# Optimization experiments

Measured on AMD Instinct MI355X. Metric: run time of the kernel, lower is better.

Reference implementation:

```python
import jax, jax.numpy as jnp
import numpy as np

DIM = 1028


def setup_inputs() -> dict:
    key = jax.random.key(0)
    ks = jax.random.split(key, 11)
    B, N = 8, 2048
    s = 0.02
    x = jax.random.normal(ks[0], (B, N, DIM), dtype=jnp.float32)
    Wq = jax.random.normal(ks[1], (DIM, DIM), dtype=jnp.float32) * s
    bq = jax.random.normal(ks[2], (DIM,), dtype=jnp.float32) * s
    Wk = jax.random.normal(ks[3], (DIM, DIM), dtype=jnp.float32) * s
    bk = jax.random.normal(ks[4], (DIM,), dtype=jnp.float32) * s
    Wv = jax.random.normal(ks[5], (DIM, DIM), dtype=jnp.float32) * s
    bv = jax.random.normal(ks[6], (DIM,), dtype=jnp.float32) * s
    We = jax.random.normal(ks[7], (4 * DIM, DIM), dtype=jnp.float32) * s
    be = jax.random.normal(ks[8], (4 * DIM,), dtype=jnp.float32) * s
    Wo = jax.random.normal(ks[9], (DIM, 4 * DIM), dtype=jnp.float32) * s
    bo = jax.random.normal(ks[10], (DIM,), dtype=jnp.float32) * s
    return {"x": x, "Wq": Wq, "bq": bq, "Wk": Wk, "bk": bk, "Wv": Wv,
            "bv": bv, "We": We, "be": be, "Wo": Wo, "bo": bo}


def reference(x, Wq, bq, Wk, bk, Wv, bv, We, be, Wo, bo):
    # x: [B, N, D]. torch Linear weight is [out, in] -> x @ W.T + b
    q = jnp.einsum('bnd,ed->bne', x, Wq) + bq
    k = jnp.einsum('bnd,ed->bne', x, Wk) + bk
    v = jnp.einsum('bnd,ed->bne', x, Wv) + bv
    scores = jnp.einsum('bqd,bkd->bqk', q, k) / jnp.sqrt(jnp.float32(DIM))
    w = jax.nn.softmax(scores, axis=-1)          # [B, N, N]
    attn = jnp.einsum('bqk,bkd->bqd', w, v)      # [B, N, D]
    h = jax.nn.gelu(jnp.einsum('bnd,hd->bnh', attn, We) + be, approximate=False)
    out = jnp.einsum('bnh,dh->bnd', h, Wo) + bo
    return out + x
```

## Files before the change

### kernel.cpp

```cpp
#include <hip/hip_runtime.h>
#include <hip/hip_bf16.h>
#include <cstdint>
#include <cmath>


typedef __bf16 bf16;
typedef __bf16 bf16x8 __attribute__((ext_vector_type(8)));
typedef float  f32x4  __attribute__((ext_vector_type(4)));

#define D_REAL   1028
#define D_PADK   1088
#define D_PADN   1152
#define H_REAL   4112
#define H_PAD    4224
#define NTOK     2048
#define NB       8
#define MTOT     (NB*NTOK)
#define SLAB_X   ((size_t)NTOK*D_PADK)
#define SLAB_S   ((size_t)NTOK*NTOK)
#define WSLAB    ((size_t)D_PADN*D_PADK)
#define VSLAB    ((size_t)D_PADN*NTOK)

__device__ __forceinline__ void async16(const void* g, void* l) {
    __builtin_amdgcn_global_load_lds(
        (__attribute__((address_space(1))) void*)(uintptr_t)g,
        (__attribute__((address_space(3))) void*)(uint32_t)(uintptr_t)l,
        16, 0, 0);
}

template <int EPI, bool XPIN>
__global__ __launch_bounds__(256)
void gemm_bt(const bf16* __restrict__ A, size_t strideA,
             const bf16* __restrict__ B, size_t strideB,
             const float* __restrict__ bias, size_t strideBias,
             void* __restrict__ Out, size_t strideOut,
             bf16* __restrict__ OutV,
             int K, int outPitch, int colBound, float scale,
             const float* __restrict__ resid)
{
    __shared__ __attribute__((aligned(16))) bf16 tA[128 * 64];
    __shared__ __attribute__((aligned(16))) bf16 tB[128 * 64];

    int bx, by, bz;
    if (XPIN) { bz = blockIdx.x; by = blockIdx.y; bx = blockIdx.z; }
    else      { bx = blockIdx.x; by = blockIdx.y; bz = blockIdx.z; }

    A += (size_t)bz * strideA;
    B += (size_t)bz * strideB;
    if (bias) bias += (size_t)bz * strideBias;

    const int tid  = threadIdx.x;
    const int lane = tid & 63;
    const int wv   = tid >> 6;
    const int wm   = wv >> 1;
    const int wn   = wv & 1;

    f32x4 acc[4][4] = {};

    const int sRow = lane >> 3;
    const int sCh  = (lane & 7) ^ sRow;
    const bf16* gA = A + (size_t)(by * 128 + wv * 32 + sRow) * K + sCh * 8;
    const bf16* gB = B + (size_t)(bx * 128 + wv * 32 + sRow) * K + sCh * 8;
    bf16* lA = &tA[(wv * 32) * 64];
    bf16* lB = &tB[(wv * 32) * 64];

    const int lr  = lane & 15;
    const int lq  = lane >> 4;
    const int rsw = lr & 7;

    for (int k0 = 0; k0 < K; k0 += 64) {
        async16(gA,                  lA);
        async16(gA + (size_t) 8 * K, lA +  8 * 64);
        async16(gA + (size_t)16 * K, lA + 16 * 64);
        async16(gA + (size_t)24 * K, lA + 24 * 64);
        async16(gB,                  lB);
        async16(gB + (size_t) 8 * K, lB +  8 * 64);
        async16(gB + (size_t)16 * K, lB + 16 * 64);
        async16(gB + (size_t)24 * K, lB + 24 * 64);
        gA += 64; gB += 64;
        __syncthreads();

        #pragma unroll
        for (int kk = 0; kk < 2; ++kk) {
            const int sl = ((kk * 4 + lq) ^ rsw) << 3;
            bf16x8 af[4], bfr[4];
            #pragma unroll
            for (int i = 0; i < 4; ++i) {
                af[i]  = *(const bf16x8*)&tA[(wm * 64 + i * 16 + lr) * 64 + sl];
                bfr[i] = *(const bf16x8*)&tB[(wn * 64 + i * 16 + lr) * 64 + sl];
            }
            #pragma unroll
            for (int i = 0; i < 4; ++i)
                #pragma unroll
                for (int j = 0; j < 4; ++j)
                    acc[i][j] = __builtin_amdgcn_mfma_f32_16x16x32_bf16(
                        af[i], bfr[j], acc[i][j], 0, 0, 0);
        }
        __syncthreads();
    }

    #pragma unroll
    for (int i = 0; i < 4; ++i) {
        #pragma unroll
        for (int j = 0; j < 4; ++j) {
            f32x4 v = acc[i][j];
            const int cg = bx * 128 + wn * 64 + j * 16 + lr;
            if (cg >= colBound) continue;
            const int rowBase = by * 128 + wm * 64 + i * 16 + lq * 4;
            const float bs = bias ? bias[cg] : 0.0f;
            #pragma unroll
            for (int r = 0; r < 4; ++r) {
                const int mg = rowBase + r;
                const float val = v[r];
                if (EPI == 0) {
                    ((bf16*)Out + (size_t)bz * strideOut)[(size_t)mg * outPitch + cg] =
                        (bf16)(val + bs);
                } else if (EPI == 3) {
                    const float u = val + bs;
                    const float g = 0.5f * u * (1.0f + erff(u * 0.70710678118654752f));
                    ((bf16*)Out)[(size_t)mg * outPitch + cg] = (bf16)g;
                } else if (EPI == 4) {
                    ((float*)Out)[(size_t)mg * outPitch + cg] =
                        val + bs + resid[(size_t)mg * outPitch + cg];
                } else if (EPI == 5) {
                    const int grp = cg / D_PADN;
                    const int c   = cg - grp * D_PADN;
                    const float u = val + bs;
                    if (grp < 2) {
                        if (c < D_PADK)
                            ((bf16*)Out)[(size_t)bz * 2 * SLAB_X + (size_t)grp * SLAB_X +
                                         (size_t)mg * D_PADK + c] = (bf16)u;
                    } else {
                        OutV[(size_t)bz * VSLAB + (size_t)c * NTOK + mg] = (bf16)u;
                    }
                } else {
                    ((bf16*)Out + (size_t)bz * strideOut)[(size_t)mg * outPitch + cg] =
                        (bf16)(val * scale);
                }
            }
        }
    }
}

__global__ __launch_bounds__(256)
void cvt_pad(const float* __restrict__ src, int R, int C,
             bf16* __restrict__ dst, int CP)
{
    const int c = blockIdx.x * 256 + threadIdx.x;
    const int r = blockIdx.y;
    if (c >= CP) return;
    const float v = (r < R && c < C) ? src[(size_t)r * C + c] : 0.0f;
    dst[(size_t)r * CP + c] = (bf16)v;
}

__global__ __launch_bounds__(256)
void pad_bias(const float* __restrict__ src, int n, float* __restrict__ dst, int np)
{
    const int i = blockIdx.x * 256 + threadIdx.x;
    if (i < np) dst[i] = (i < n) ? src[i] : 0.0f;
}

__global__ __launch_bounds__(256)
void softmax_ip(bf16* __restrict__ S)
{
    const int row  = blockIdx.x * 4 + (threadIdx.x >> 6);
    const int lane = threadIdx.x & 63;
    bf16* s = S + (size_t)row * NTOK + lane * 8;

    float v[32];
    #pragma unroll
    for (int j = 0; j < 4; ++j) {
        bf16x8 t = *(const bf16x8*)(s + j * 512);
        #pragma unroll
        for (int e = 0; e < 8; ++e) v[j * 8 + e] = (float)t[e];
    }
    float m = -1e30f;
    #pragma unroll
    for (int i = 0; i < 32; ++i) m = fmaxf(m, v[i]);
    #pragma unroll
    for (int off = 32; off > 0; off >>= 1) m = fmaxf(m, __shfl_xor(m, off, 64));

    float sum = 0.0f;
    #pragma unroll
    for (int i = 0; i < 32; ++i) { v[i] = __expf(v[i] - m); sum += v[i]; }
    #pragma unroll
    for (int off = 32; off > 0; off >>= 1) sum += __shfl_xor(sum, off, 64);
    const float inv = 1.0f / sum;

    #pragma unroll
    for (int j = 0; j < 4; ++j) {
        bf16x8 t;
        #pragma unroll
        for (int e = 0; e < 8; ++e) t[e] = (bf16)(v[j * 8 + e] * inv);
        *(bf16x8*)(s + j * 512) = t;
    }
}

#define OFF_WQKV   0u
#define OFF_WE     7520256u
#define OFF_WO     16711680u
#define OFF_BQKV   26443776u
#define OFF_BE     26457600u
#define OFF_XBF    26474496u
#define OFF_VT     62126080u
#define OFF_SCR    99874816u
#define QS_BYTES   8912896u
#define SS_BYTES   8388608u

extern "C" void kernel_launch(void* const* d_in, const int* in_sizes, int n_in,
                              void* d_out, int out_size, void* d_ws, size_t ws_size,
                              hipStream_t stream)
{
    const float* x  = (const float*)d_in[0];
    const float* Wq = (const float*)d_in[1];
    const float* bq = (const float*)d_in[2];
    const float* Wk = (const float*)d_in[3];
    const float* bk = (const float*)d_in[4];
    const float* Wv = (const float*)d_in[5];
    const float* bv = (const float*)d_in[6];
    const float* We = (const float*)d_in[7];
    const float* be = (const float*)d_in[8];
    const float* Wo = (const float*)d_in[9];
    const float* bo = (const float*)d_in[10];

    char* ws = (char*)d_ws;
    bf16*  Wqkv = (bf16*)(ws + OFF_WQKV);
    bf16*  WeP  = (bf16*)(ws + OFF_WE);
    bf16*  WoP  = (bf16*)(ws + OFF_WO);
    float* Bqkv = (float*)(ws + OFF_BQKV);
    float* BeP  = (float*)(ws + OFF_BE);
    bf16*  Xbf  = (bf16*)(ws + OFF_XBF);
    bf16*  Vt   = (bf16*)(ws + OFF_VT);
    char*  scr  = ws + OFF_SCR;

    const size_t avail = ws_size > OFF_SCR ? ws_size - OFF_SCR : 0;
    const size_t perG  = (size_t)QS_BYTES + SS_BYTES;
    int G = (avail >= 8 * perG) ? 8 : (avail >= 4 * perG) ? 4
          : (avail >= 2 * perG) ? 2 : 1;
    int R = (avail >= 69206016u) ? 8192 : (avail >= 34603008u) ? 4096 : 2048;

    bf16* Qs = (bf16*)scr;
    bf16* Ss = (bf16*)(scr + (size_t)G * QS_BYTES);
    bf16* Hb = (bf16*)scr;

    const dim3 blk(256);
    const float inv_sqrt_d = (float)(1.0 / sqrt((double)D_REAL));

    cvt_pad<<<dim3(5, MTOT), blk, 0, stream>>>(x, MTOT, D_REAL, Xbf, D_PADK);
    cvt_pad<<<dim3(5, D_PADN), blk, 0, stream>>>(Wq, D_REAL, D_REAL, Wqkv, D_PADK);
    cvt_pad<<<dim3(5, D_PADN), blk, 0, stream>>>(Wk, D_REAL, D_REAL, Wqkv + WSLAB, D_PADK);
    cvt_pad<<<dim3(5, D_PADN), blk, 0, stream>>>(Wv, D_REAL, D_REAL, Wqkv + 2 * WSLAB, D_PADK);
    cvt_pad<<<dim3(5, H_PAD), blk, 0, stream>>>(We, H_REAL, D_REAL, WeP, D_PADK);
    cvt_pad<<<dim3(17, D_PADN), blk, 0, stream>>>(Wo, D_REAL, H_REAL, WoP, H_PAD);
    pad_bias<<<dim3(5), blk, 0, stream>>>(bq, D_REAL, Bqkv, D_PADN);
    pad_bias<<<dim3(5), blk, 0, stream>>>(bk, D_REAL, Bqkv + D_PADN, D_PADN);
    pad_bias<<<dim3(5), blk, 0, stream>>>(bv, D_REAL, Bqkv + 2 * D_PADN, D_PADN);
    pad_bias<<<dim3(17), blk, 0, stream>>>(be, H_REAL, BeP, H_PAD);

    for (int g0 = 0; g0 < NB; g0 += G) {
        gemm_bt<5, false><<<dim3(27, 16, G), blk, 0, stream>>>(
            Xbf + (size_t)g0 * SLAB_X, SLAB_X, Wqkv, 0, Bqkv, 0,
            Qs, 0, Vt + (size_t)g0 * VSLAB,
            D_PADK, 0, 3456, 1.0f, nullptr);
        gemm_bt<6, true><<<dim3(G, 16, 16), blk, 0, stream>>>(
            Qs, 2 * SLAB_X, Qs + SLAB_X, 2 * SLAB_X, nullptr, 0,
            Ss, SLAB_S, nullptr, D_PADK, NTOK, NTOK, inv_sqrt_d, nullptr);
        softmax_ip<<<dim3(G * 512), blk, 0, stream>>>(Ss);
        gemm_bt<0, true><<<dim3(G, 16, 9), blk, 0, stream>>>(
            Ss, SLAB_S, Vt + (size_t)g0 * VSLAB, VSLAB, nullptr, 0,
            Xbf + (size_t)g0 * SLAB_X, SLAB_X, nullptr,
            NTOK, D_PADK, D_PADK, 1.0f, nullptr);
    }

    for (int r0 = 0; r0 < MTOT; r0 += R) {
        gemm_bt<3, false><<<dim3(33, R / 128, 1), blk, 0, stream>>>(
            Xbf + (size_t)r0 * D_PADK, 0, WeP, 0, BeP, 0,
            Hb, 0, nullptr, D_PADK, H_PAD, H_PAD, 1.0f, nullptr);
        gemm_bt<4, false><<<dim3(9, R / 128, 1), blk, 0, stream>>>(
            Hb, 0, WoP, 0, bo, 0,
            (float*)d_out + (size_t)r0 * D_REAL, 0, nullptr,
            H_PAD, D_REAL, D_REAL, 1.0f, x + (size_t)r0 * D_REAL);
    }
}
```

Before: 1.069 ms.

## Replace 128x128 GEMM with 256x256 double-buffered 512-thread pipelined kernel

Replaces the single-buffered 128x128 GEMM with a 256x256 tile kernel that runs 8 waves. It double-buffers A and B in LDS, issues async global-to-LDS loads for later k-tiles between MFMA phases, and raises wave priority during MFMA bursts. Non-pinned grids also get an XCD-aware block remap. The aim is more reuse of each loaded tile, and hiding load latency behind MFMA work. In exchange it uses 128KB of LDS per block, which limits occupancy. Edge tiles read past padded weight and V rows, relying on column guards to discard the results.

```diff
diff --git a/kernel.cpp b/kernel.cpp
--- a/kernel.cpp
+++ b/kernel.cpp
@@ -28,9 +28,11 @@
         16, 0, 0);
 }
 
+#define MFMA_(a, b, c) __builtin_amdgcn_mfma_f32_16x16x32_bf16(a, b, c, 0, 0, 0)
+
 template <int EPI, bool XPIN>
-__global__ __launch_bounds__(256)
-void gemm_bt(const bf16* __restrict__ A, size_t strideA,
+__global__ __launch_bounds__(512, 2)
+void gemm256(const bf16* __restrict__ A, size_t strideA,
              const bf16* __restrict__ B, size_t strideB,
              const float* __restrict__ bias, size_t strideBias,
              void* __restrict__ Out, size_t strideOut,
@@ -38,12 +40,19 @@
              int K, int outPitch, int colBound, float scale,
              const float* __restrict__ resid)
 {
-    __shared__ __attribute__((aligned(16))) bf16 tA[128 * 64];
-    __shared__ __attribute__((aligned(16))) bf16 tB[128 * 64];
+    __shared__ __attribute__((aligned(16))) bf16 sAB[4][256 * 64];
 
     int bx, by, bz;
-    if (XPIN) { bz = blockIdx.x; by = blockIdx.y; bx = blockIdx.z; }
-    else      { bx = blockIdx.x; by = blockIdx.y; bz = blockIdx.z; }
+    if (XPIN) {
+        bz = blockIdx.x; by = blockIdx.y; bx = blockIdx.z;
+    } else {
+        const int nx   = gridDim.x;
+        const int nwg  = nx * gridDim.y;
+        const int orig = blockIdx.y * nx + blockIdx.x;
+        const int q    = nwg >> 3;
+        const int wg   = (orig & 7) * q + (orig >> 3);
+        bx = wg % nx; by = wg / nx; bz = blockIdx.z;
+    }
 
     A += (size_t)bz * strideA;
     B += (size_t)bz * strideB;
@@ -52,61 +61,127 @@
     const int tid  = threadIdx.x;
     const int lane = tid & 63;
     const int wv   = tid >> 6;
-    const int wm   = wv >> 1;
-    const int wn   = wv & 1;
-
-    f32x4 acc[4][4] = {};
-
-    const int sRow = lane >> 3;
-    const int sCh  = (lane & 7) ^ sRow;
-    const bf16* gA = A + (size_t)(by * 128 + wv * 32 + sRow) * K + sCh * 8;
-    const bf16* gB = B + (size_t)(bx * 128 + wv * 32 + sRow) * K + sCh * 8;
-    bf16* lA = &tA[(wv * 32) * 64];
-    bf16* lB = &tB[(wv * 32) * 64];
-
-    const int lr  = lane & 15;
-    const int lq  = lane >> 4;
-    const int rsw = lr & 7;
-
-    for (int k0 = 0; k0 < K; k0 += 64) {
-        async16(gA,                  lA);
-        async16(gA + (size_t) 8 * K, lA +  8 * 64);
-        async16(gA + (size_t)16 * K, lA + 16 * 64);
-        async16(gA + (size_t)24 * K, lA + 24 * 64);
-        async16(gB,                  lB);
-        async16(gB + (size_t) 8 * K, lB +  8 * 64);
-        async16(gB + (size_t)16 * K, lB + 16 * 64);
-        async16(gB + (size_t)24 * K, lB + 24 * 64);
-        gA += 64; gB += 64;
-        __syncthreads();
-
-        #pragma unroll
-        for (int kk = 0; kk < 2; ++kk) {
-            const int sl = ((kk * 4 + lq) ^ rsw) << 3;
-            bf16x8 af[4], bfr[4];
-            #pragma unroll
-            for (int i = 0; i < 4; ++i) {
-                af[i]  = *(const bf16x8*)&tA[(wm * 64 + i * 16 + lr) * 64 + sl];
-                bfr[i] = *(const bf16x8*)&tB[(wn * 64 + i * 16 + lr) * 64 + sl];
-            }
-            #pragma unroll
-            for (int i = 0; i < 4; ++i)
-                #pragma unroll
-                for (int j = 0; j < 4; ++j)
-                    acc[i][j] = __builtin_amdgcn_mfma_f32_16x16x32_bf16(
-                        af[i], bfr[j], acc[i][j], 0, 0, 0);
-        }
-        __syncthreads();
-    }
-
-    #pragma unroll
-    for (int i = 0; i < 4; ++i) {
+    const int wm   = wv >> 2;
+    const int wn   = wv & 3;
+
+    const int    NT  = K >> 6;
+    const size_t K64 = (size_t)K * 64;
+
+    const int sRow = tid >> 3;
+    const int sCh  = (tid & 7) ^ (sRow & 7);
+    const bf16* gA = A + (size_t)(by * 256 + sRow) * K + sCh * 8;
+    const bf16* gB = B + (size_t)(bx * 256 + sRow) * K + sCh * 8;
+    const int ldsOff = sRow * 64 + (tid & 7) * 8;
+
+#define STAGE_A(tt) do {                                           \
+        const bf16* g_ = gA + (size_t)(tt) * 64;                   \
+        bf16* l_ = &sAB[(tt) & 1][0] + ldsOff;                     \
+        async16(g_,           l_);                                 \
+        async16(g_ +     K64, l_ +  4096);                         \
+        async16(g_ + 2 * K64, l_ +  8192);                         \
+        async16(g_ + 3 * K64, l_ + 12288);                         \
+    } while (0)
+#define STAGE_B_HALF(tt, h) do {                                   \
+        const bf16* g_ = gB + (size_t)(tt) * 64 + (2 * (h)) * K64; \
+        bf16* l_ = &sAB[2 + ((tt) & 1)][0] + ldsOff + (2*(h))*4096;\
+        async16(g_,       l_);                                     \
+        async16(g_ + K64, l_ + 4096);                              \
+    } while (0)
+
+    const int lr   = lane & 15;
+    const int lq   = lane >> 4;
+    const int rsw  = lr & 7;
+    const int aRow = (wm * 128 + lr) * 64;
+    const int bRow = (wn * 64  + lr) * 64;
+    const int sl0  = (lq ^ rsw) << 3;
+    const int sl1  = ((lq + 4) ^ rsw) << 3;
+
+#define LDA_(i, s) (*(const bf16x8*)&sAc[aRow + (i) * 1024 + (s)])
+#define LDB_(j, s) (*(const bf16x8*)&sBc[bRow + (j) * 1024 + (s)])
+
+    f32x4 acc[8][4] = {};
+
+#define MM(i, a0, a1) do {                                  \
+        acc[i][0] = MFMA_(a0, bfr[0][0], acc[i][0]);        \
+        acc[i][0] = MFMA_(a1, bfr[0][1], acc[i][0]);        \
+        acc[i][1] = MFMA_(a0, bfr[1][0], acc[i][1]);        \
+        acc[i][1] = MFMA_(a1, bfr[1][1], acc[i][1]);        \
+        acc[i][2] = MFMA_(a0, bfr[2][0], acc[i][2]);        \
+        acc[i][2] = MFMA_(a1, bfr[2][1], acc[i][2]);        \
+        acc[i][3] = MFMA_(a0, bfr[3][0], acc[i][3]);        \
+        acc[i][3] = MFMA_(a1, bfr[3][1], acc[i][3]);        \
+    } while (0)
+
+#define PH_ENTER() do {                                          \
+        __builtin_amdgcn_s_barrier();                            \
+        asm volatile("s_waitcnt lgkmcnt(0)" ::: "memory");       \
+        __builtin_amdgcn_sched_barrier(0);                       \
+        __builtin_amdgcn_s_setprio(1);                           \
+    } while (0)
+#define PH_EXIT() do {                                           \
+        __builtin_amdgcn_s_setprio(0);                           \
+        __builtin_amdgcn_s_barrier();                            \
+    } while (0)
+
+    STAGE_A(0); STAGE_B_HALF(0, 0); STAGE_B_HALF(0, 1);
+    STAGE_A(1); STAGE_B_HALF(1, 0); STAGE_B_HALF(1, 1);
+    asm volatile("s_waitcnt vmcnt(8)" ::: "memory");
+    __builtin_amdgcn_s_barrier();
+
+    for (int t = 0; t < NT; ++t) {
+        const int bcur = t & 1;
+        const bf16* sAc = sAB[bcur];
+        const bf16* sBc = sAB[2 + bcur];
+        bf16x8 bfr[4][2];
+        bf16x8 aA, aB, aC, aD;
+
+        bfr[0][0] = LDB_(0, sl0); bfr[0][1] = LDB_(0, sl1);
+        bfr[1][0] = LDB_(1, sl0); bfr[1][1] = LDB_(1, sl1);
+        bfr[2][0] = LDB_(2, sl0); bfr[2][1] = LDB_(2, sl1);
+        bfr[3][0] = LDB_(3, sl0); bfr[3][1] = LDB_(3, sl1);
+        aA = LDA_(0, sl0); aB = LDA_(0, sl1);
+        aC = LDA_(1, sl0); aD = LDA_(1, sl1);
+        if (t >= 1 && t + 1 < NT) STAGE_A(t + 1);
+        PH_ENTER();
+        MM(0, aA, aB); MM(1, aC, aD);
+        PH_EXIT();
+
+        aA = LDA_(2, sl0); aB = LDA_(2, sl1);
+        aC = LDA_(3, sl0); aD = LDA_(3, sl1);
+        if (t + 2 < NT) STAGE_B_HALF(t + 2, 0);
+        PH_ENTER();
+        MM(2, aA, aB); MM(3, aC, aD);
+        PH_EXIT();
+
+        aA = LDA_(4, sl0); aB = LDA_(4, sl1);
+        aC = LDA_(5, sl0); aD = LDA_(5, sl1);
+        if (t + 2 < NT) STAGE_B_HALF(t + 2, 1);
+        PH_ENTER();
+        MM(4, aA, aB); MM(5, aC, aD);
+        PH_EXIT();
+
+        aA = LDA_(6, sl0); aB = LDA_(6, sl1);
+        aC = LDA_(7, sl0); aD = LDA_(7, sl1);
+        __builtin_amdgcn_s_barrier();
+        asm volatile("s_waitcnt lgkmcnt(0)" ::: "memory");
+        __builtin_amdgcn_sched_barrier(0);
+        __builtin_amdgcn_s_setprio(1);
+        MM(6, aA, aB); MM(7, aC, aD);
+        __builtin_amdgcn_s_setprio(0);
+        if (t + 2 < NT)       asm volatile("s_waitcnt vmcnt(4)" ::: "memory");
+        else if (t + 2 == NT) asm volatile("s_waitcnt vmcnt(0)" ::: "memory");
+        __builtin_amdgcn_s_barrier();
+        __builtin_amdgcn_sched_barrier(0);
+    }
+
+    #pragma unroll
+    for (int i = 0; i < 8; ++i) {
+        const int rowBase = by * 256 + wm * 128 + i * 16 + lq * 4;
         #pragma unroll
         for (int j = 0; j < 4; ++j) {
             f32x4 v = acc[i][j];
-            const int cg = bx * 128 + wn * 64 + j * 16 + lr;
+            const int cg = bx * 256 + wn * 64 + j * 16 + lr;
             if (cg >= colBound) continue;
-            const int rowBase = by * 128 + wm * 64 + i * 16 + lq * 4;
             const float bs = bias ? bias[cg] : 0.0f;
             #pragma unroll
             for (int r = 0; r < 4; ++r) {
@@ -140,6 +215,13 @@
             }
         }
     }
+#undef STAGE_A
+#undef STAGE_B_HALF
+#undef LDA_
+#undef LDB_
+#undef MM
+#undef PH_ENTER
+#undef PH_EXIT
 }
 
 __global__ __launch_bounds__(256)
@@ -244,6 +326,7 @@
     bf16* Hb = (bf16*)scr;
 
     const dim3 blk(256);
+    const dim3 blkG(512);
     const float inv_sqrt_d = (float)(1.0 / sqrt((double)D_REAL));
 
     cvt_pad<<<dim3(5, MTOT), blk, 0, stream>>>(x, MTOT, D_REAL, Xbf, D_PADK);
@@ -258,25 +341,25 @@
     pad_bias<<<dim3(17), blk, 0, stream>>>(be, H_REAL, BeP, H_PAD);
 
     for (int g0 = 0; g0 < NB; g0 += G) {
-        gemm_bt<5, false><<<dim3(27, 16, G), blk, 0, stream>>>(
+        gemm256<5, false><<<dim3(14, 8, G), blkG, 0, stream>>>(
             Xbf + (size_t)g0 * SLAB_X, SLAB_X, Wqkv, 0, Bqkv, 0,
             Qs, 0, Vt + (size_t)g0 * VSLAB,
             D_PADK, 0, 3456, 1.0f, nullptr);
-        gemm_bt<6, true><<<dim3(G, 16, 16), blk, 0, stream>>>(
+        gemm256<6, true><<<dim3(G, 8, 8), blkG, 0, stream>>>(
             Qs, 2 * SLAB_X, Qs + SLAB_X, 2 * SLAB_X, nullptr, 0,
             Ss, SLAB_S, nullptr, D_PADK, NTOK, NTOK, inv_sqrt_d, nullptr);
         softmax_ip<<<dim3(G * 512), blk, 0, stream>>>(Ss);
-        gemm_bt<0, true><<<dim3(G, 16, 9), blk, 0, stream>>>(
+        gemm256<0, true><<<dim3(G, 8, 5), blkG, 0, stream>>>(
             Ss, SLAB_S, Vt + (size_t)g0 * VSLAB, VSLAB, nullptr, 0,
             Xbf + (size_t)g0 * SLAB_X, SLAB_X, nullptr,
             NTOK, D_PADK, D_PADK, 1.0f, nullptr);
     }
 
     for (int r0 = 0; r0 < MTOT; r0 += R) {
-        gemm_bt<3, false><<<dim3(33, R / 128, 1), blk, 0, stream>>>(
+        gemm256<3, false><<<dim3(17, R / 256, 1), blkG, 0, stream>>>(
             Xbf + (size_t)r0 * D_PADK, 0, WeP, 0, BeP, 0,
             Hb, 0, nullptr, D_PADK, H_PAD, H_PAD, 1.0f, nullptr);
-        gemm_bt<4, false><<<dim3(9, R / 128, 1), blk, 0, stream>>>(
+        gemm256<4, false><<<dim3(5, R / 256, 1), blkG, 0, stream>>>(
             Hb, 0, WoP, 0, bo, 0,
             (float*)d_out + (size_t)r0 * D_REAL, 0, nullptr,
             H_PAD, D_REAL, D_REAL, 1.0f, x + (size_t)r0 * D_REAL);
```

After: 1.149 ms. 7.5% more time.
